# Optimization experiments

Hardware: AMD Instinct MI355X
Metric: run time of the kernel (lower is better)

Reference implementation:

```python
import jax, jax.numpy as jnp
import numpy as np

B_SZ = 16
IN_CH = 4
OUT_CH = 256          # d_model
KSIZE = 16
STRIDE = 8
L_IN = 20000
D_STATE = 128
EXPAND = 2
D_INNER = EXPAND * OUT_CH            # 512
HEADDIM = 64
NHEADS = D_INNER // HEADDIM          # 8
D_CONV = 4
NGROUPS = 1
L_CONV = (L_IN - KSIZE) // STRIDE + 1  # 2499
FLAT = STRIDE * L_CONV                 # 19992 == Config.INPUT_LENGTH
CHUNK = 128
DN = ('NCH', 'OIH', 'NCH')


def setup_inputs() -> dict:
    key = jax.random.key(0)
    ks = jax.random.split(key, 20)
    r = lambda i, shape, s=0.02: jax.random.normal(ks[i], shape, jnp.float32) * s
    return {
        'x': jax.random.normal(ks[0], (B_SZ, IN_CH, L_IN), jnp.float32),
        'conv_w': r(1, (OUT_CH, IN_CH, KSIZE), 0.1),
        'conv_b': r(2, (OUT_CH,), 0.1),
        'bn_w': jnp.ones((OUT_CH,), jnp.float32),
        'bn_b': jnp.zeros((OUT_CH,), jnp.float32),
        'in_proj_w': r(3, (2 * D_INNER + 2 * NGROUPS * D_STATE + NHEADS, OUT_CH)),
        'conv1d_w': r(4, (D_INNER + 2 * NGROUPS * D_STATE, 1, D_CONV), 0.2),
        'conv1d_b': r(5, (D_INNER + 2 * NGROUPS * D_STATE,), 0.1),
        'dt_bias': jnp.linspace(-4.0, -1.0, NHEADS, dtype=jnp.float32),
        'A_log': jnp.log(jnp.arange(1, NHEADS + 1, dtype=jnp.float32)),
        'D': r(6, (NHEADS,), 0.5) + 1.0,
        'norm_w': jnp.ones((D_INNER,), jnp.float32),
        'out_proj_w': r(7, (OUT_CH, D_INNER)),
        'conv1_w': r(8, (STRIDE, OUT_CH, KSIZE), 0.05),
        'conv1_b': r(9, (STRIDE,), 0.1),
        'w1': r(10, (512, FLAT)), 'b1': jnp.zeros((512,), jnp.float32),
        'w2': r(11, (256, 512), 0.05), 'b2': jnp.zeros((256,), jnp.float32),
        'w3': r(12, (64, 256), 0.05), 'b3': jnp.zeros((64,), jnp.float32),
        'w4': r(13, (1, 64), 0.05), 'b4': jnp.zeros((1,), jnp.float32),
    }


def _segsum(a):
    # a: [..., q] -> [..., q, q]; entry (i,j) = sum_{k=j+1..i} a_k on lower triangle
    q = a.shape[-1]
    cs = jnp.cumsum(a, axis=-1)
    seg = cs[..., :, None] - cs[..., None, :]
    mask = jnp.tril(jnp.ones((q, q), dtype=bool))
    return jnp.where(mask, seg, -jnp.inf)


def _ssd(xw, dA, Bm, Cm, chunk):
    # Chunked SSD (Mamba2): xw = dt-weighted inputs [b,l,h,p]; dA = dt*A [b,l,h];
    # Bm, Cm: [b,l,n]. Causal; zero-padding at the tail cannot affect y[:, :l].
    b, l, h, p = xw.shape
    n = Bm.shape[-1]
    pad = (-l) % chunk
    xw = jnp.pad(xw, ((0, 0), (0, pad), (0, 0), (0, 0)))
    dA = jnp.pad(dA, ((0, 0), (0, pad), (0, 0)))
    Bm = jnp.pad(Bm, ((0, 0), (0, pad), (0, 0)))
    Cm = jnp.pad(Cm, ((0, 0), (0, pad), (0, 0)))
    c = (l + pad) // chunk
    xw = xw.reshape(b, c, chunk, h, p)
    dA = dA.reshape(b, c, chunk, h).transpose(0, 3, 1, 2)   # [b,h,c,q]
    Bm = Bm.reshape(b, c, chunk, n)
    Cm = Cm.reshape(b, c, chunk, n)
    Acs = jnp.cumsum(dA, axis=-1)                            # [b,h,c,q]
    Ldiag = jnp.exp(_segsum(dA))                             # [b,h,c,q,q]
    Ydiag = jnp.einsum('bcln,bcsn,bhcls,bcshp->bclhp', Cm, Bm, Ldiag, xw)
    decay_states = jnp.exp(Acs[..., -1:] - Acs)              # [b,h,c,q]
    states = jnp.einsum('bcln,bhcl,bclhp->bchpn', Bm, decay_states, xw)
    chunk_decay = jnp.exp(Acs[..., -1])                      # [b,h,c]

    def step(carry, inp):
        s, d = inp
        return carry * d[..., None, None] + s, carry

    init = jnp.zeros((b, h, p, n), xw.dtype)
    _, prev = jax.lax.scan(step, init,
                           (states.transpose(1, 0, 2, 3, 4),
                            chunk_decay.transpose(2, 0, 1)))
    prev = prev.transpose(1, 0, 2, 3, 4)                     # [b,c,h,p,n]
    Yoff = jnp.einsum('bcln,bchpn,bhcl->bclhp', Cm, prev, jnp.exp(Acs))
    return (Ydiag + Yoff).reshape(b, l + pad, h, p)[:, :l]


def reference(x, conv_w, conv_b, bn_w, bn_b, in_proj_w, conv1d_w, conv1d_b,
              dt_bias, A_log, D, norm_w, out_proj_w, conv1_w, conv1_b,
              w1, b1, w2, b2, w3, b3, w4, b4):
    # conv -> BN (batch stats, training-mode math) -> ReLU
    h = jax.lax.conv_general_dilated(x, conv_w, (STRIDE,), 'VALID',
                                     dimension_numbers=DN) + conv_b[None, :, None]
    mean = h.mean(axis=(0, 2), keepdims=True)
    var = h.var(axis=(0, 2), keepdims=True)
    h = (h - mean) * jax.lax.rsqrt(var + 1e-5)
    h = jax.nn.relu(h * bn_w[None, :, None] + bn_b[None, :, None])
    u = h.transpose(0, 2, 1)                                 # [b, l, d_model]

    # ---- Mamba2 block ----
    zxbcdt = u @ in_proj_w.T                                 # [b, l, 1288]
    z, xBC, dt = jnp.split(zxbcdt, [D_INNER, 2 * D_INNER + 2 * NGROUPS * D_STATE], axis=-1)
    # causal depthwise conv1d over xBC + SiLU
    xBC_t = jnp.pad(xBC.transpose(0, 2, 1), ((0, 0), (0, 0), (D_CONV - 1, 0)))
    xBC_t = jax.lax.conv_general_dilated(xBC_t, conv1d_w, (1,), 'VALID',
                                         dimension_numbers=DN,
                                         feature_group_count=xBC.shape[-1])
    xBC = jax.nn.silu((xBC_t + conv1d_b[None, :, None]).transpose(0, 2, 1))
    xm, Bm, Cm = jnp.split(xBC, [D_INNER, D_INNER + NGROUPS * D_STATE], axis=-1)
    dt = jax.nn.softplus(dt + dt_bias)                       # [b, l, nheads]
    A = -jnp.exp(A_log)                                      # [nheads]
    xh = xm.reshape(xm.shape[0], xm.shape[1], NHEADS, HEADDIM)
    y = _ssd(xh * dt[..., None], dt * A, Bm, Cm, CHUNK)
    y = y + D[None, None, :, None] * xh                      # D skip
    y = y.reshape(y.shape[0], y.shape[1], D_INNER)
    # gated RMSNorm (norm_before_gate=False): rmsnorm(y * silu(z)) * w
    y = y * jax.nn.silu(z)
    y = y * jax.lax.rsqrt(jnp.mean(y * y, axis=-1, keepdims=True) + 1e-5) * norm_w
    y = y @ out_proj_w.T                                     # [b, l, d_model]

    # conv1 with padding='same' (PyTorch: left=(k-1)//2, right=k-1-left)
    h = y.transpose(0, 2, 1)
    pad_l = (KSIZE - 1) // 2
    h = jax.lax.conv_general_dilated(h, conv1_w, (1,), [(pad_l, KSIZE - 1 - pad_l)],
                                     dimension_numbers=DN) + conv1_b[None, :, None]
    f = h.reshape(h.shape[0], -1)                            # [b, 8*2499=19992]
    f = jax.nn.relu(f @ w1.T + b1)
    f = jax.nn.relu(f @ w2.T + b2)
    f = jax.nn.relu(f @ w3.T + b3)
    return f @ w4.T + b4                                     # [b, 1]
```

## Files before the change

kernel.cpp:

```cpp
#include <hip/hip_runtime.h>
#include <math.h>

constexpr int B    = 16;
constexpr int L    = 2499;
constexpr int DIN  = 512;
constexpr int NH   = 8;
constexpr int DS   = 128;
constexpr int NC   = 20;
constexpr int XBCD = 768;
constexpr int FLAT = 19992;
constexpr int FLATP= 20000;
constexpr long ROWS = (long)B * L;

constexpr size_t S_DTV  = 0;
constexpr size_t S_CS   = 1279488;
constexpr size_t S_STAT = 2590208;
constexpr size_t S_WPK  = 2594304;
constexpr size_t S_HALO = 2725376;
constexpr size_t OFF_HT  = 4199936;
constexpr size_t OFF_XBC = 24671744;
constexpr size_t OFF_CBST= 86087168;
constexpr size_t CB_OFF  = 0;
constexpr size_t ST_OFF  = 5242880;
constexpr size_t Z_OFF   = 0;
constexpr size_t F_OFF   = 0;
constexpr size_t O1A_OFF = 640000;
constexpr size_t O1_OFF  = 672768;
constexpr size_t O2_OFF  = 705536;
constexpr size_t O3_OFF  = 721920;
constexpr size_t W1B_OFF = 726016;
constexpr size_t WS_NEEDED = 127030784;

typedef unsigned short u16;
typedef __attribute__((ext_vector_type(8))) short bf16x8;
typedef __attribute__((ext_vector_type(4))) float f32x4;

__device__ __forceinline__ float bf2f(unsigned int u) {
    return __uint_as_float(u << 16);
}
__device__ __forceinline__ u16 f2bf(float f) {
    unsigned int x = __float_as_uint(f);
    unsigned int r = x + 0x7fffu + ((x >> 16) & 1u);
    return (u16)(r >> 16);
}
__device__ __forceinline__ unsigned int pk2(float a, float b) {
    return (unsigned int)f2bf(a) | ((unsigned int)f2bf(b) << 16);
}
__device__ __forceinline__ void ld8bf(const u16* p, float* o) {
    uint4 v = *(const uint4*)p;
    o[0]=bf2f(v.x&0xffffu); o[1]=bf2f(v.x>>16);
    o[2]=bf2f(v.y&0xffffu); o[3]=bf2f(v.y>>16);
    o[4]=bf2f(v.z&0xffffu); o[5]=bf2f(v.z>>16);
    o[6]=bf2f(v.w&0xffffu); o[7]=bf2f(v.w>>16);
}
__device__ __forceinline__ void ld4bf(const u16* p, float* o) {
    uint2 v = *(const uint2*)p;
    o[0]=bf2f(v.x&0xffffu); o[1]=bf2f(v.x>>16);
    o[2]=bf2f(v.y&0xffffu); o[3]=bf2f(v.y>>16);
}
__device__ __forceinline__ void st8bf(u16* p, const float* s) {
    uint4 v;
    v.x = pk2(s[0],s[1]); v.y = pk2(s[2],s[3]);
    v.z = pk2(s[4],s[5]); v.w = pk2(s[6],s[7]);
    *(uint4*)p = v;
}
__device__ __forceinline__ float siluf(float x) { return x / (1.f + expf(-x)); }

__global__ __launch_bounds__(256) void k_zero(float* __restrict__ p, int n) {
    int i = blockIdx.x * 256 + threadIdx.x;
    if (i < n) p[i] = 0.f;
}

__global__ __launch_bounds__(256) void k_wcvt(const float* __restrict__ src,
                                              u16* __restrict__ dst, int n) {
    int i = blockIdx.x * 256 + threadIdx.x;
    if (i < n) dst[i] = f2bf(src[i]);
}

__global__ __launch_bounds__(256) void k_w1cvt(const float* __restrict__ w1,
                                               u16* __restrict__ w1b) {
    long e0 = ((long)blockIdx.x * 256 + threadIdx.x) * 8;
    int n = (int)(e0 / FLATP);
    int k = (int)(e0 - (long)n * FLATP);
    const float* src = w1 + (long)n * FLAT + k;
    u16* dst = w1b + e0;
    if (k + 8 <= FLAT) {
        float4 a = *(const float4*)src;
        float4 b = *(const float4*)(src + 4);
        *(uint4*)dst = (uint4){pk2(a.x,a.y), pk2(a.z,a.w), pk2(b.x,b.y), pk2(b.z,b.w)};
    } else {
        #pragma unroll
        for (int i = 0; i < 8; ++i)
            dst[i] = (k + i < FLAT) ? f2bf(src[i]) : (u16)0;
    }
}

template <bool IM2COL, bool BF16OUT>
__global__ __launch_bounds__(256) void gemm_mfma(const void* __restrict__ Ap,
                                                 const u16* __restrict__ Wb,
                                                 void* __restrict__ Cp,
                                                 int M, int N, int K, int lda, int ldc) {
    __shared__ u16 Als[128 * 40];
    __shared__ u16 Bls[128 * 40];
    int tid = threadIdx.x;
    int wave = tid >> 6, lane = tid & 63;
    int wr = wave >> 1, wc = wave & 1;
    int m0 = blockIdx.x * 128, n0 = blockIdx.y * 128;
    int l15 = lane & 15, l4 = lane >> 4;
    int srow = tid >> 1, scol = (tid & 1) * 16;

    f32x4 acc[4][4];
    #pragma unroll
    for (int i = 0; i < 4; ++i)
        #pragma unroll
        for (int j = 0; j < 4; ++j)
            acc[i][j] = (f32x4){0.f, 0.f, 0.f, 0.f};

    for (int k0 = 0; k0 < K; k0 += 32) {
        {
            int am = m0 + srow;
            uint4 v0 = {0,0,0,0}, v1 = {0,0,0,0};
            if (am < M) {
                if (IM2COL) {
                    const float* x = (const float*)Ap;
                    int b = am / L, l = am - b * L;
                    int ic = (k0 + scol) >> 4;
                    const float* px = x + ((long)(b * 4 + ic)) * 20000 + l * 8;
                    float4 f0 = *(const float4*)(px);
                    float4 f1 = *(const float4*)(px + 4);
                    float4 f2 = *(const float4*)(px + 8);
                    float4 f3 = *(const float4*)(px + 12);
                    v0.x = pk2(f0.x,f0.y); v0.y = pk2(f0.z,f0.w);
                    v0.z = pk2(f1.x,f1.y); v0.w = pk2(f1.z,f1.w);
                    v1.x = pk2(f2.x,f2.y); v1.y = pk2(f2.z,f2.w);
                    v1.z = pk2(f3.x,f3.y); v1.w = pk2(f3.z,f3.w);
                } else {
                    const u16* pa = (const u16*)Ap + (long)am * lda + k0 + scol;
                    v0 = *(const uint4*)pa;
                    v1 = *(const uint4*)(pa + 8);
                }
            }
            *(uint4*)&Als[srow * 40 + scol]     = v0;
            *(uint4*)&Als[srow * 40 + scol + 8] = v1;
        }
        {
            const u16* pw = Wb + (long)(n0 + srow) * K + k0 + scol;
            *(uint4*)&Bls[srow * 40 + scol]     = *(const uint4*)pw;
            *(uint4*)&Bls[srow * 40 + scol + 8] = *(const uint4*)(pw + 8);
        }
        __syncthreads();

        bf16x8 af[4], bfr[4];
        #pragma unroll
        for (int i = 0; i < 4; ++i) {
            af[i]  = *(const bf16x8*)&Als[(wr * 64 + i * 16 + l15) * 40 + l4 * 8];
            bfr[i] = *(const bf16x8*)&Bls[(wc * 64 + i * 16 + l15) * 40 + l4 * 8];
        }
        #pragma unroll
        for (int i = 0; i < 4; ++i)
            #pragma unroll
            for (int j = 0; j < 4; ++j)
                acc[i][j] = __builtin_amdgcn_mfma_f32_16x16x32_bf16(
                    af[i], bfr[j], acc[i][j], 0, 0, 0);
        __syncthreads();
    }

    #pragma unroll
    for (int i = 0; i < 4; ++i) {
        #pragma unroll
        for (int j = 0; j < 4; ++j) {
            int n = n0 + wc * 64 + j * 16 + l15;
            #pragma unroll
            for (int r = 0; r < 4; ++r) {
                int m = m0 + wr * 64 + i * 16 + l4 * 4 + r;
                if (m < M) {
                    if (BF16OUT) ((u16*)Cp)[(long)m * ldc + n] = f2bf(acc[i][j][r]);
                    else         ((float*)Cp)[(long)m * ldc + n] = acc[i][j][r];
                }
            }
        }
    }
}

__global__ __launch_bounds__(256) void k_bnstats(const u16* __restrict__ h,
                                                 float* __restrict__ sums,
                                                 float* __restrict__ sumsq) {
    int c = threadIdx.x;
    float s = 0.f, s2 = 0.f;
    for (long r = blockIdx.x; r < ROWS; r += gridDim.x) {
        float v = bf2f(h[r * 256 + c]);
        s += v; s2 += v * v;
    }
    atomicAdd(&sums[c], s);
    atomicAdd(&sumsq[c], s2);
}

__global__ __launch_bounds__(256) void k_bnfinal(const float* __restrict__ sums,
                                                 const float* __restrict__ sumsq,
                                                 const float* __restrict__ bn_w,
                                                 const float* __restrict__ bn_b,
                                                 float* __restrict__ scale,
                                                 float* __restrict__ shift) {
    int c = threadIdx.x;
    float mean = sums[c] / (float)ROWS;
    float var  = sumsq[c] / (float)ROWS - mean * mean;
    float inv  = rsqrtf(var + 1e-5f);
    float sc   = bn_w[c] * inv;
    scale[c] = sc;
    shift[c] = bn_b[c] - mean * sc;
}

__global__ __launch_bounds__(256) void k_bnapply(u16* __restrict__ ht,
                                                 const float* __restrict__ scale,
                                                 const float* __restrict__ shift) {
    long i = ((long)blockIdx.x * 256 + threadIdx.x) * 8;
    int c = (int)(i & 255);
    float v[8];
    ld8bf(ht + i, v);
    float4 s0 = *(const float4*)(scale + c), s1 = *(const float4*)(scale + c + 4);
    float4 h0 = *(const float4*)(shift + c), h1 = *(const float4*)(shift + c + 4);
    v[0]=fmaxf(fmaf(v[0],s0.x,h0.x),0.f); v[1]=fmaxf(fmaf(v[1],s0.y,h0.y),0.f);
    v[2]=fmaxf(fmaf(v[2],s0.z,h0.z),0.f); v[3]=fmaxf(fmaf(v[3],s0.w,h0.w),0.f);
    v[4]=fmaxf(fmaf(v[4],s1.x,h1.x),0.f); v[5]=fmaxf(fmaf(v[5],s1.y,h1.y),0.f);
    v[6]=fmaxf(fmaf(v[6],s1.z,h1.z),0.f); v[7]=fmaxf(fmaf(v[7],s1.w,h1.w),0.f);
    st8bf(ht + i, v);
}

__global__ __launch_bounds__(256) void k_dtproj(const u16* __restrict__ u,
                                                const float* __restrict__ in_proj_w,
                                                const float* __restrict__ dt_bias,
                                                float* __restrict__ dtv) {
    long idx = (long)blockIdx.x * 256 + threadIdx.x;
    if (idx >= ROWS * 8) return;
    int h = (int)(idx & 7);
    long row = idx >> 3;
    const float* wr = in_proj_w + (long)(1280 + h) * 256;
    const u16* ar = u + row * 256;
    float acc = dt_bias[h];
    for (int k = 0; k < 256; ++k)
        acc = fmaf(bf2f(ar[k]), wr[k], acc);
    dtv[idx] = (acc > 20.f) ? acc : log1pf(expf(acc));
}

__global__ __launch_bounds__(256) void k_halo(const u16* __restrict__ xbc,
                                              u16* __restrict__ halo) {
    long idx = (long)blockIdx.x * 256 + threadIdx.x;
    if (idx >= 16L * 19 * 3 * 768) return;
    int ch = (int)(idx % 768);
    long t1 = idx / 768;
    int j = (int)(t1 % 3);
    long t2 = t1 / 3;
    int t = (int)(t2 % 19) + 1;
    int b = (int)(t2 / 19);
    halo[(((long)b * 20 + t) * 3 + j) * 768 + ch] =
        xbc[((long)b * L + t * 128 - 3 + j) * 768 + ch];
}

__global__ __launch_bounds__(256) void k_dwip(u16* __restrict__ xbc,
                                              const u16* __restrict__ halo,
                                              const float* __restrict__ w,
                                              const float* __restrict__ bias) {
    int cg = blockIdx.x % 3;
    int t  = (blockIdx.x / 3) % 20;
    int b  = blockIdx.x / 60;
    int ch = cg * 256 + threadIdx.x;
    int l0 = t * 128, l1 = min(l0 + 128, L);
    float W0 = w[ch*4+0], W1 = w[ch*4+1], W2 = w[ch*4+2], W3 = w[ch*4+3];
    float bs = bias[ch];
    float p0 = 0.f, p1 = 0.f, p2 = 0.f;
    if (t > 0) {
        const u16* hp = halo + (((long)b * 20 + t) * 3) * 768 + ch;
        p0 = bf2f(hp[0]); p1 = bf2f(hp[768]); p2 = bf2f(hp[1536]);
    }
    u16* base = xbc + ((long)b * L + l0) * 768 + ch;
    for (int l = l0; l < l1; ++l) {
        float p3 = bf2f(*base);
        float acc = fmaf(p0, W0, fmaf(p1, W1, fmaf(p2, W2, fmaf(p3, W3, bs))));
        *base = f2bf(siluf(acc));
        p0 = p1; p1 = p2; p2 = p3;
        base += 768;
    }
}

__global__ __launch_bounds__(128) void k_cs(const float* __restrict__ dtv,
                                            const float* __restrict__ A_log,
                                            float* __restrict__ cs) {
    int c = blockIdx.x % NC;
    int h = (blockIdx.x / NC) % NH;
    int b = blockIdx.x / (NC * NH);
    int q = threadIdx.x;
    int lg = c * 128 + q;
    float Av = -expf(A_log[h]);
    float dA = 0.f;
    if (lg < L) dA = dtv[((long)b * L + lg) * 8 + h] * Av;
    __shared__ float buf[128];
    buf[q] = dA;
    __syncthreads();
    for (int off = 1; off < 128; off <<= 1) {
        float add = (q >= off) ? buf[q - off] : 0.f;
        __syncthreads();
        buf[q] += add;
        __syncthreads();
    }
    cs[(long)blockIdx.x * 128 + q] = buf[q];
}

__global__ __launch_bounds__(256) void k_cb(const u16* __restrict__ xbc,
                                            u16* __restrict__ cb, int bo) {
    int c = blockIdx.x % NC, bl = blockIdx.x / NC;
    int b = bo + bl;
    long bcl = blockIdx.x;
    __shared__ u16 Als[128 * 40];
    __shared__ u16 Bls[128 * 40];
    int tid = threadIdx.x;
    int wave = tid >> 6, lane = tid & 63;
    int wr = wave >> 1, wc = wave & 1;
    int l15 = lane & 15, l4 = lane >> 4;
    int srow = tid >> 1, scol = (tid & 1) * 16;

    f32x4 acc[4][4];
    #pragma unroll
    for (int i = 0; i < 4; ++i)
        #pragma unroll
        for (int j = 0; j < 4; ++j)
            acc[i][j] = (f32x4){0.f, 0.f, 0.f, 0.f};

    int lg = c * 128 + srow;
    const u16* prow = xbc + ((long)b * L + lg) * XBCD;

    for (int k0 = 0; k0 < 128; k0 += 32) {
        uint4 cv0 = {0,0,0,0}, cv1 = cv0, bv0 = cv0, bv1 = cv0;
        if (lg < L) {
            cv0 = *(const uint4*)(prow + 640 + k0 + scol);
            cv1 = *(const uint4*)(prow + 640 + k0 + scol + 8);
            bv0 = *(const uint4*)(prow + 512 + k0 + scol);
            bv1 = *(const uint4*)(prow + 512 + k0 + scol + 8);
        }
        *(uint4*)&Als[srow * 40 + scol]     = cv0;
        *(uint4*)&Als[srow * 40 + scol + 8] = cv1;
        *(uint4*)&Bls[srow * 40 + scol]     = bv0;
        *(uint4*)&Bls[srow * 40 + scol + 8] = bv1;
        __syncthreads();

        bf16x8 af[4], bfr[4];
        #pragma unroll
        for (int i = 0; i < 4; ++i) {
            af[i]  = *(const bf16x8*)&Als[(wr * 64 + i * 16 + l15) * 40 + l4 * 8];
            bfr[i] = *(const bf16x8*)&Bls[(wc * 64 + i * 16 + l15) * 40 + l4 * 8];
        }
        #pragma unroll
        for (int i = 0; i < 4; ++i)
            #pragma unroll
            for (int j = 0; j < 4; ++j)
                acc[i][j] = __builtin_amdgcn_mfma_f32_16x16x32_bf16(
                    af[i], bfr[j], acc[i][j], 0, 0, 0);
        __syncthreads();
    }

    #pragma unroll
    for (int i = 0; i < 4; ++i)
        #pragma unroll
        for (int j = 0; j < 4; ++j) {
            int n = wc * 64 + j * 16 + l15;
            #pragma unroll
            for (int r = 0; r < 4; ++r) {
                int m = wr * 64 + i * 16 + l4 * 4 + r;
                cb[(bcl * 128 + m) * 128 + n] = f2bf(acc[i][j][r]);
            }
        }
}

__global__ __launch_bounds__(256) void k_states(const u16* __restrict__ xbc,
                                                const float* __restrict__ dtv,
                                                const float* __restrict__ cs,
                                                u16* __restrict__ st, int bo) {
    int h = blockIdx.x & 7;
    int c = (blockIdx.x >> 3) % NC;
    int bl = blockIdx.x / (8 * NC);
    int b = bo + bl;
    __shared__ u16 At[128][136];
    __shared__ u16 Bt[64][136];
    long csbase = (((long)b * 8 + h) * NC + c) * 128;
    float csLast = cs[csbase + 127];
    int tid = threadIdx.x;
    int lane = tid & 63, wave = tid >> 6;
    int wr = wave >> 1, wc = wave & 1;
    int l15 = lane & 15, l4 = lane >> 4;

    int l0 = 2 * (tid & 63), l1 = l0 + 1;
    int q = tid >> 6;
    int lg0 = c * 128 + l0, lg1 = c * 128 + l1;
    long row0 = (long)b * L + lg0, row1 = row0 + 1;
    float wl0 = 0.f, wl1 = 0.f, dt0 = 0.f, dt1 = 0.f;
    if (lg0 < L) { wl0 = expf(csLast - cs[csbase + l0]); dt0 = dtv[row0 * 8 + h]; }
    if (lg1 < L) { wl1 = expf(csLast - cs[csbase + l1]); dt1 = dtv[row1 * 8 + h]; }

    #pragma unroll
    for (int nb = 0; nb < 4; ++nb) {
        int n0 = q * 32 + nb * 8;
        float a0[8] = {0,0,0,0,0,0,0,0}, a1[8] = {0,0,0,0,0,0,0,0};
        if (lg0 < L) ld8bf(xbc + row0 * XBCD + 512 + n0, a0);
        if (lg1 < L) ld8bf(xbc + row1 * XBCD + 512 + n0, a1);
        #pragma unroll
        for (int i = 0; i < 8; ++i)
            *(unsigned int*)&At[n0 + i][l0] = pk2(a0[i] * wl0, a1[i] * wl1);
    }
    #pragma unroll
    for (int pb = 0; pb < 2; ++pb) {
        int p0 = q * 16 + pb * 8;
        float a0[8] = {0,0,0,0,0,0,0,0}, a1[8] = {0,0,0,0,0,0,0,0};
        if (lg0 < L) ld8bf(xbc + row0 * XBCD + h * 64 + p0, a0);
        if (lg1 < L) ld8bf(xbc + row1 * XBCD + h * 64 + p0, a1);
        #pragma unroll
        for (int i = 0; i < 8; ++i)
            *(unsigned int*)&Bt[p0 + i][l0] = pk2(a0[i] * dt0, a1[i] * dt1);
    }
    __syncthreads();

    f32x4 acc[4][2];
    #pragma unroll
    for (int i = 0; i < 4; ++i)
        #pragma unroll
        for (int j = 0; j < 2; ++j)
            acc[i][j] = (f32x4){0.f, 0.f, 0.f, 0.f};

    #pragma unroll
    for (int k0 = 0; k0 < 128; k0 += 32) {
        bf16x8 af[4], bfr[2];
        #pragma unroll
        for (int i = 0; i < 4; ++i)
            af[i] = *(const bf16x8*)&At[wr * 64 + i * 16 + l15][k0 + l4 * 8];
        #pragma unroll
        for (int j = 0; j < 2; ++j)
            bfr[j] = *(const bf16x8*)&Bt[wc * 32 + j * 16 + l15][k0 + l4 * 8];
        #pragma unroll
        for (int i = 0; i < 4; ++i)
            #pragma unroll
            for (int j = 0; j < 2; ++j)
                acc[i][j] = __builtin_amdgcn_mfma_f32_16x16x32_bf16(
                    af[i], bfr[j], acc[i][j], 0, 0, 0);
    }

    long basep = (long)blockIdx.x * 8192;
    #pragma unroll
    for (int i = 0; i < 4; ++i)
        #pragma unroll
        for (int j = 0; j < 2; ++j) {
            int p = wc * 32 + j * 16 + l15;
            #pragma unroll
            for (int r = 0; r < 4; ++r) {
                int n = wr * 64 + i * 16 + l4 * 4 + r;
                st[basep + n * 64 + p] = f2bf(acc[i][j][r]);
            }
        }
}

__global__ __launch_bounds__(256) void k_scan(const float* __restrict__ cs,
                                              u16* __restrict__ st, int bo) {
    int h = blockIdx.x & 7, bl = (blockIdx.x >> 3) & 7, q = blockIdx.x >> 6;
    int b = bo + bl;
    int tid = threadIdx.x;
    float carry[8];
    #pragma unroll
    for (int i = 0; i < 8; ++i) carry[i] = 0.f;
    long csbase = ((long)b * 8 + h) * NC * 128;
    for (int c = 0; c < NC; ++c) {
        float cd = expf(cs[csbase + c * 128 + 127]);
        u16* p = st + (((long)bl * NC + c) * 8 + h) * 8192 + q * 2048;
        #pragma unroll
        for (int i = 0; i < 8; ++i) {
            int e = tid + i * 256;
            float v = bf2f(p[e]);
            p[e] = f2bf(carry[i]);
            carry[i] = carry[i] * cd + v;
        }
    }
}

__global__ __launch_bounds__(256) void k_yout(u16* __restrict__ xbc,
                                              const float* __restrict__ dtv,
                                              const float* __restrict__ cs,
                                              const u16* __restrict__ cb,
                                              const u16* __restrict__ st,
                                              const float* __restrict__ Dv, int bo) {
    int h = blockIdx.x & 7;
    int c = (blockIdx.x >> 3) % NC;
    int bl = blockIdx.x / (8 * NC);
    int b = bo + bl;
    long bcl = (long)bl * NC + c;
    __shared__ u16 Am[128][136];
    __shared__ u16 Bt[64][136];
    __shared__ float csb[128], ecs[128];
    int tid = threadIdx.x;
    long csbase = (((long)b * 8 + h) * NC + c) * 128;
    if (tid < 128) {
        float v = cs[csbase + tid];
        csb[tid] = v;
        ecs[tid] = expf(v);
    }
    __syncthreads();

    int lane = tid & 63, wave = tid >> 6;
    int wr = wave >> 1, wc = wave & 1;
    int l15 = lane & 15, l4 = lane >> 4;
    int lrow = tid >> 1, sh = (tid & 1) * 64;
    int l0 = 2 * (tid & 63), l1 = l0 + 1;
    int q = tid >> 6;
    int lg0 = c * 128 + l0, lg1 = c * 128 + l1;
    long row0 = (long)b * L + lg0, row1 = row0 + 1;

    {
        float cl = csb[lrow];
        const u16* cbrow = cb + (bcl * 128 + lrow) * 128;
        #pragma unroll
        for (int sb = 0; sb < 8; ++sb) {
            int s0 = sh + sb * 8;
            float a[8];
            ld8bf(cbrow + s0, a);
            #pragma unroll
            for (int i = 0; i < 8; ++i) {
                int s = s0 + i;
                float w = (s <= lrow) ? expf(cl - csb[s]) : 0.f;
                a[i] *= w;
            }
            st8bf(&Am[lrow][s0], a);
        }
        float dt0 = 0.f, dt1 = 0.f;
        if (lg0 < L) dt0 = dtv[row0 * 8 + h];
        if (lg1 < L) dt1 = dtv[row1 * 8 + h];
        #pragma unroll
        for (int pb = 0; pb < 2; ++pb) {
            int p0 = q * 16 + pb * 8;
            float a0[8] = {0,0,0,0,0,0,0,0}, a1[8] = {0,0,0,0,0,0,0,0};
            if (lg0 < L) ld8bf(xbc + row0 * XBCD + h * 64 + p0, a0);
            if (lg1 < L) ld8bf(xbc + row1 * XBCD + h * 64 + p0, a1);
            #pragma unroll
            for (int i = 0; i < 8; ++i)
                *(unsigned int*)&Bt[p0 + i][l0] = pk2(a0[i] * dt0, a1[i] * dt1);
        }
    }
    __syncthreads();

    f32x4 acc[4][2];
    #pragma unroll
    for (int i = 0; i < 4; ++i)
        #pragma unroll
        for (int j = 0; j < 2; ++j)
            acc[i][j] = (f32x4){0.f, 0.f, 0.f, 0.f};

    #pragma unroll
    for (int k0 = 0; k0 < 128; k0 += 32) {
        bf16x8 af[4], bfr[2];
        #pragma unroll
        for (int i = 0; i < 4; ++i)
            af[i] = *(const bf16x8*)&Am[wr * 64 + i * 16 + l15][k0 + l4 * 8];
        #pragma unroll
        for (int j = 0; j < 2; ++j)
            bfr[j] = *(const bf16x8*)&Bt[wc * 32 + j * 16 + l15][k0 + l4 * 8];
        #pragma unroll
        for (int i = 0; i < 4; ++i)
            #pragma unroll
            for (int j = 0; j < 2; ++j)
                acc[i][j] = __builtin_amdgcn_mfma_f32_16x16x32_bf16(
                    af[i], bfr[j], acc[i][j], 0, 0, 0);
    }
    __syncthreads();

    {
        float el = ecs[lrow];
        int lgr = c * 128 + lrow;
        const u16* xr = xbc + ((long)b * L + lgr) * XBCD + 640;
        #pragma unroll
        for (int nb = 0; nb < 8; ++nb) {
            int n0 = sh + nb * 8;
            float a[8] = {0,0,0,0,0,0,0,0};
            if (lgr < L) {
                ld8bf(xr + n0, a);
                #pragma unroll
                for (int i = 0; i < 8; ++i) a[i] *= el;
            }
            st8bf(&Am[lrow][n0], a);
        }
        const u16* pv = st + (bcl * 8 + h) * 8192;
        #pragma unroll
        for (int pb = 0; pb < 2; ++pb) {
            int p0 = q * 16 + pb * 8;
            float a0[8], a1[8];
            ld8bf(pv + (long)l0 * 64 + p0, a0);
            ld8bf(pv + (long)l1 * 64 + p0, a1);
            #pragma unroll
            for (int i = 0; i < 8; ++i)
                *(unsigned int*)&Bt[p0 + i][l0] = pk2(a0[i], a1[i]);
        }
    }
    __syncthreads();

    #pragma unroll
    for (int k0 = 0; k0 < 128; k0 += 32) {
        bf16x8 af[4], bfr[2];
        #pragma unroll
        for (int i = 0; i < 4; ++i)
            af[i] = *(const bf16x8*)&Am[wr * 64 + i * 16 + l15][k0 + l4 * 8];
        #pragma unroll
        for (int j = 0; j < 2; ++j)
            bfr[j] = *(const bf16x8*)&Bt[wc * 32 + j * 16 + l15][k0 + l4 * 8];
        #pragma unroll
        for (int i = 0; i < 4; ++i)
            #pragma unroll
            for (int j = 0; j < 2; ++j)
                acc[i][j] = __builtin_amdgcn_mfma_f32_16x16x32_bf16(
                    af[i], bfr[j], acc[i][j], 0, 0, 0);
    }

    float Dh = Dv[h];
    #pragma unroll
    for (int i = 0; i < 4; ++i)
        #pragma unroll
        for (int r = 0; r < 4; ++r) {
            int l = wr * 64 + i * 16 + l4 * 4 + r;
            int lg = c * 128 + l;
            if (lg >= L) continue;
            long row = (long)b * L + lg;
            #pragma unroll
            for (int j = 0; j < 2; ++j) {
                int p = wc * 32 + j * 16 + l15;
                u16* xp = xbc + row * XBCD + h * 64 + p;
                float xv = bf2f(*xp);
                *xp = f2bf(fmaf(Dh, xv, acc[i][j][r]));
            }
        }
}

__global__ __launch_bounds__(256) void k_rmsnorm(u16* __restrict__ y,
                                                 const u16* __restrict__ z,
                                                 const float* __restrict__ nw) {
    long r = blockIdx.x;
    int tid = threadIdx.x;
    float v0 = bf2f(y[r * XBCD + tid]), v1 = bf2f(y[r * XBCD + 256 + tid]);
    float z0 = bf2f(z[r * DIN + tid]),  z1 = bf2f(z[r * DIN + 256 + tid]);
    v0 *= siluf(z0);
    v1 *= siluf(z1);
    __shared__ float red[256];
    red[tid] = v0 * v0 + v1 * v1;
    __syncthreads();
    for (int s = 128; s > 0; s >>= 1) {
        if (tid < s) red[tid] += red[tid + s];
        __syncthreads();
    }
    float sc = rsqrtf(red[0] / 512.f + 1e-5f);
    y[r * XBCD + tid]       = f2bf(v0 * sc * nw[tid]);
    y[r * XBCD + 256 + tid] = f2bf(v1 * sc * nw[256 + tid]);
}

__global__ __launch_bounds__(256) void k_wpack(const float* __restrict__ w,
                                               u16* __restrict__ wp) {
    int idx = blockIdx.x * 256 + threadIdx.x;
    if (idx >= 8 * 256 * 16) return;
    int k = idx & 15;
    int cidx = (idx >> 4) & 255;
    int s = idx >> 12;
    wp[(s * 16 + k) * 256 + cidx] = f2bf(w[idx]);
}

__global__ __launch_bounds__(256) void k_conv1(const u16* __restrict__ G,
                                               const float* __restrict__ bias,
                                               u16* __restrict__ f) {
    long idx = (long)blockIdx.x * 256 + threadIdx.x;
    if (idx >= (long)B * 8 * L) {
        long j = idx - (long)B * 8 * L;
        if (j < 16 * 8)
            f[(j >> 3) * FLATP + FLAT + (j & 7)] = 0;
        return;
    }
    int l = (int)(idx % L);
    long t = idx / L;
    int s = (int)(t & 7);
    int b = (int)(t >> 3);
    float acc = bias[s];
    #pragma unroll
    for (int k = 0; k < 16; ++k) {
        int ls = l + k - 7;
        if (ls >= 0 && ls < L)
            acc += bf2f(G[((long)b * L + ls) * 128 + s * 16 + k]);
    }
    f[(long)b * FLATP + s * L + l] = f2bf(acc);
}

__global__ __launch_bounds__(256) void k_mlp1(const u16* __restrict__ fb,
                                              const u16* __restrict__ w1b,
                                              float* __restrict__ o1acc) {
    int wave = threadIdx.x >> 6, lane = threadIdx.x & 63;
    int l15 = lane & 15, l4 = lane >> 4;
    int n0 = blockIdx.x * 64 + wave * 16;
    int k0 = blockIdx.y * 800;
    const u16* fp = fb + (long)l15 * FLATP + k0 + l4 * 8;
    const u16* wp = w1b + (long)(n0 + l15) * FLATP + k0 + l4 * 8;
    f32x4 acc = (f32x4){0.f, 0.f, 0.f, 0.f};
    #pragma unroll
    for (int kk = 0; kk < 25; ++kk) {
        bf16x8 af = *(const bf16x8*)fp;
        bf16x8 bf = *(const bf16x8*)wp;
        acc = __builtin_amdgcn_mfma_f32_16x16x32_bf16(af, bf, acc, 0, 0, 0);
        fp += 32; wp += 32;
    }
    #pragma unroll
    for (int r = 0; r < 4; ++r) {
        int b = l4 * 4 + r;
        atomicAdd(&o1acc[b * 512 + n0 + l15], acc[r]);
    }
}

__global__ __launch_bounds__(256) void k_mlp1fin(const float* __restrict__ o1acc,
                                                 const float* __restrict__ b1,
                                                 float* __restrict__ o1) {
    int i = blockIdx.x * 256 + threadIdx.x;
    o1[i] = fmaxf(o1acc[i] + b1[i & 511], 0.f);
}

__global__ __launch_bounds__(256) void k_mlp2(const float* __restrict__ in,
                                              const float* __restrict__ w,
                                              const float* __restrict__ bias,
                                              float* __restrict__ out) {
    int b = blockIdx.x, n = threadIdx.x;
    const float* ir = in + b * 512;
    const float* wr = w + (long)n * 512;
    float acc = 0.f;
    for (int k = 0; k < 512; ++k) acc = fmaf(ir[k], wr[k], acc);
    out[b * 256 + n] = fmaxf(acc + bias[n], 0.f);
}

__global__ __launch_bounds__(64) void k_mlp3(const float* __restrict__ in,
                                             const float* __restrict__ w,
                                             const float* __restrict__ bias,
                                             float* __restrict__ out) {
    int b = blockIdx.x, n = threadIdx.x;
    const float* ir = in + b * 256;
    const float* wr = w + (long)n * 256;
    float acc = 0.f;
    for (int k = 0; k < 256; ++k) acc = fmaf(ir[k], wr[k], acc);
    out[b * 64 + n] = fmaxf(acc + bias[n], 0.f);
}

__global__ __launch_bounds__(64) void k_mlp4(const float* __restrict__ in,
                                             const float* __restrict__ w4,
                                             const float* __restrict__ b4,
                                             float* __restrict__ dout) {
    int b = blockIdx.x, k = threadIdx.x;
    float v = in[b * 64 + k] * w4[k];
    #pragma unroll
    for (int off = 32; off > 0; off >>= 1) v += __shfl_down(v, off);
    if (k == 0) dout[b] = v + b4[0];
}

extern "C" void kernel_launch(void* const* d_in, const int* in_sizes, int n_in,
                              void* d_out, int out_size, void* d_ws, size_t ws_size,
                              hipStream_t stream) {
    (void)in_sizes; (void)n_in; (void)out_size;
    if (ws_size < WS_NEEDED) return;

    const float* x         = (const float*)d_in[0];
    const float* conv_w    = (const float*)d_in[1];
    const float* bn_w      = (const float*)d_in[3];
    const float* bn_b      = (const float*)d_in[4];
    const float* in_proj_w = (const float*)d_in[5];
    const float* conv1d_w  = (const float*)d_in[6];
    const float* conv1d_b  = (const float*)d_in[7];
    const float* dt_bias   = (const float*)d_in[8];
    const float* A_log     = (const float*)d_in[9];
    const float* Dp        = (const float*)d_in[10];
    const float* norm_w    = (const float*)d_in[11];
    const float* out_proj_w= (const float*)d_in[12];
    const float* conv1_w   = (const float*)d_in[13];
    const float* conv1_b   = (const float*)d_in[14];
    const float* w1 = (const float*)d_in[15]; const float* b1 = (const float*)d_in[16];
    const float* w2 = (const float*)d_in[17]; const float* b2 = (const float*)d_in[18];
    const float* w3 = (const float*)d_in[19]; const float* b3 = (const float*)d_in[20];
    const float* w4 = (const float*)d_in[21]; const float* b4 = (const float*)d_in[22];

    char* base = (char*)d_ws;
    float* dtv  = (float*)(base + S_DTV);
    float* cs   = (float*)(base + S_CS);
    float* sums = (float*)(base + S_STAT);
    float* sumsq= sums + 256;
    float* scale= sums + 512;
    float* shift= sums + 768;
    u16*   cwbf = (u16*)(base + S_WPK);
    u16*   wbf  = (u16*)(base + S_HALO);
    u16*   halo = (u16*)(base + S_HALO);
    u16*   ht   = (u16*)(base + OFF_HT);
    u16*   xbc  = (u16*)(base + OFF_XBC);
    u16*   cb   = (u16*)(base + OFF_CBST + CB_OFF);
    u16*   st   = (u16*)(base + OFF_CBST + ST_OFF);
    u16*   zb   = (u16*)(base + OFF_CBST + Z_OFF);
    u16*   G    = (u16*)(base + OFF_XBC);
    u16*   fbuf = (u16*)(base + OFF_CBST + F_OFF);
    float* o1a  = (float*)(base + OFF_CBST + O1A_OFF);
    float* o1   = (float*)(base + OFF_CBST + O1_OFF);
    float* o2   = (float*)(base + OFF_CBST + O2_OFF);
    float* o3   = (float*)(base + OFF_CBST + O3_OFF);
    u16*   w1b  = (u16*)(base + OFF_CBST + W1B_OFF);
    u16*   yproj= ht;

    k_wcvt<<<64, 256, 0, stream>>>(conv_w, cwbf, 256 * 64);
    gemm_mfma<true, true><<<dim3(313, 2), 256, 0, stream>>>(
        x, cwbf, ht, (int)ROWS, 256, 64, 0, 256);

    k_zero<<<2, 256, 0, stream>>>(sums, 512);
    k_bnstats<<<256, 256, 0, stream>>>(ht, sums, sumsq);
    k_bnfinal<<<1, 256, 0, stream>>>(sums, sumsq, bn_w, bn_b, scale, shift);
    k_bnapply<<<4998, 256, 0, stream>>>(ht, scale, shift);

    k_wcvt<<<768, 256, 0, stream>>>(in_proj_w + 512L * 256, wbf, 768 * 256);
    gemm_mfma<false, true><<<dim3(313, 6), 256, 0, stream>>>(
        ht, wbf, xbc, (int)ROWS, 768, 256, 256, 768);
    k_dtproj<<<1250, 256, 0, stream>>>(ht, in_proj_w, dt_bias, dtv);

    k_halo<<<2736, 256, 0, stream>>>(xbc, halo);
    k_dwip<<<960, 256, 0, stream>>>(xbc, halo, conv1d_w, conv1d_b);
    k_cs<<<2560, 128, 0, stream>>>(dtv, A_log, cs);

    for (int bh = 0; bh < 2; ++bh) {
        int bo = bh * 8;
        k_cb<<<160, 256, 0, stream>>>(xbc, cb, bo);
        k_states<<<1280, 256, 0, stream>>>(xbc, dtv, cs, st, bo);
        k_scan<<<256, 256, 0, stream>>>(cs, st, bo);
        k_yout<<<1280, 256, 0, stream>>>(xbc, dtv, cs, cb, st, Dp, bo);
    }

    k_wcvt<<<512, 256, 0, stream>>>(in_proj_w, wbf, 512 * 256);
    gemm_mfma<false, true><<<dim3(313, 4), 256, 0, stream>>>(
        ht, wbf, zb, (int)ROWS, 512, 256, 256, 512);

    k_rmsnorm<<<39984, 256, 0, stream>>>(xbc, zb, norm_w);
    k_wcvt<<<512, 256, 0, stream>>>(out_proj_w, wbf, 256 * 512);
    gemm_mfma<false, true><<<dim3(313, 2), 256, 0, stream>>>(
        xbc, wbf, yproj, (int)ROWS, 256, 512, 768, 256);

    k_wpack<<<128, 256, 0, stream>>>(conv1_w, wbf);
    gemm_mfma<false, true><<<dim3(313, 1), 256, 0, stream>>>(
        yproj, wbf, G, (int)ROWS, 128, 256, 256, 128);
    k_conv1<<<1250, 256, 0, stream>>>(G, conv1_b, fbuf);

    k_w1cvt<<<5000, 256, 0, stream>>>(w1, w1b);
    k_zero<<<32, 256, 0, stream>>>(o1a, 8192);
    k_mlp1<<<dim3(8, 25), 256, 0, stream>>>(fbuf, w1b, o1a);
    k_mlp1fin<<<32, 256, 0, stream>>>(o1a, b1, o1);
    k_mlp2<<<16, 256, 0, stream>>>(o1, w2, b2, o2);
    k_mlp3<<<16, 64, 0, stream>>>(o2, w3, b3, o3);
    k_mlp4<<<16, 64, 0, stream>>>(o3, w4, b4, (float*)d_out);
}
```

Before: 709.9 us.

## Halve SSD shared tiles via K-split, use exp2 cumsums, wave-per-row RMSNorm

```diff
diff --git a/kernel.cpp b/kernel.cpp
--- a/kernel.cpp
+++ b/kernel.cpp
@@ -11,6 +11,7 @@
 constexpr int FLAT = 19992;
 constexpr int FLATP= 20000;
 constexpr long ROWS = (long)B * L;
+constexpr float LOG2E = 1.4426950408889634f;
 
 constexpr size_t S_DTV  = 0;
 constexpr size_t S_CS   = 1279488;
@@ -302,7 +303,7 @@
         buf[q] += add;
         __syncthreads();
     }
-    cs[(long)blockIdx.x * 128 + q] = buf[q];
+    cs[(long)blockIdx.x * 128 + q] = buf[q] * LOG2E;
 }
 
 __global__ __launch_bounds__(256) void k_cb(const u16* __restrict__ xbc,
@@ -378,44 +379,15 @@
     int c = (blockIdx.x >> 3) % NC;
     int bl = blockIdx.x / (8 * NC);
     int b = bo + bl;
-    __shared__ u16 At[128][136];
-    __shared__ u16 Bt[64][136];
+    __shared__ u16 At[128][72];
+    __shared__ u16 Bt[64][72];
     long csbase = (((long)b * 8 + h) * NC + c) * 128;
-    float csLast = cs[csbase + 127];
+    float cs2Last = cs[csbase + 127];
     int tid = threadIdx.x;
     int lane = tid & 63, wave = tid >> 6;
     int wr = wave >> 1, wc = wave & 1;
     int l15 = lane & 15, l4 = lane >> 4;
-
-    int l0 = 2 * (tid & 63), l1 = l0 + 1;
-    int q = tid >> 6;
-    int lg0 = c * 128 + l0, lg1 = c * 128 + l1;
-    long row0 = (long)b * L + lg0, row1 = row0 + 1;
-    float wl0 = 0.f, wl1 = 0.f, dt0 = 0.f, dt1 = 0.f;
-    if (lg0 < L) { wl0 = expf(csLast - cs[csbase + l0]); dt0 = dtv[row0 * 8 + h]; }
-    if (lg1 < L) { wl1 = expf(csLast - cs[csbase + l1]); dt1 = dtv[row1 * 8 + h]; }
-
-    #pragma unroll
-    for (int nb = 0; nb < 4; ++nb) {
-        int n0 = q * 32 + nb * 8;
-        float a0[8] = {0,0,0,0,0,0,0,0}, a1[8] = {0,0,0,0,0,0,0,0};
-        if (lg0 < L) ld8bf(xbc + row0 * XBCD + 512 + n0, a0);
-        if (lg1 < L) ld8bf(xbc + row1 * XBCD + 512 + n0, a1);
-        #pragma unroll
-        for (int i = 0; i < 8; ++i)
-            *(unsigned int*)&At[n0 + i][l0] = pk2(a0[i] * wl0, a1[i] * wl1);
-    }
-    #pragma unroll
-    for (int pb = 0; pb < 2; ++pb) {
-        int p0 = q * 16 + pb * 8;
-        float a0[8] = {0,0,0,0,0,0,0,0}, a1[8] = {0,0,0,0,0,0,0,0};
-        if (lg0 < L) ld8bf(xbc + row0 * XBCD + h * 64 + p0, a0);
-        if (lg1 < L) ld8bf(xbc + row1 * XBCD + h * 64 + p0, a1);
-        #pragma unroll
-        for (int i = 0; i < 8; ++i)
-            *(unsigned int*)&Bt[p0 + i][l0] = pk2(a0[i] * dt0, a1[i] * dt1);
-    }
-    __syncthreads();
+    int pr = tid & 31, grp = tid >> 5;
 
     f32x4 acc[4][2];
     #pragma unroll
@@ -425,20 +397,52 @@
             acc[i][j] = (f32x4){0.f, 0.f, 0.f, 0.f};
 
     #pragma unroll
-    for (int k0 = 0; k0 < 128; k0 += 32) {
-        bf16x8 af[4], bfr[2];
-        #pragma unroll
-        for (int i = 0; i < 4; ++i)
-            af[i] = *(const bf16x8*)&At[wr * 64 + i * 16 + l15][k0 + l4 * 8];
-        #pragma unroll
-        for (int j = 0; j < 2; ++j)
-            bfr[j] = *(const bf16x8*)&Bt[wc * 32 + j * 16 + l15][k0 + l4 * 8];
-        #pragma unroll
-        for (int i = 0; i < 4; ++i)
+    for (int lh = 0; lh < 2; ++lh) {
+        int l0 = lh * 64 + 2 * pr, l1 = l0 + 1;
+        int lg0 = c * 128 + l0, lg1 = lg0 + 1;
+        long row0 = (long)b * L + lg0, row1 = row0 + 1;
+        float wl0 = 0.f, wl1 = 0.f, dt0 = 0.f, dt1 = 0.f;
+        if (lg0 < L) { wl0 = exp2f(cs2Last - cs[csbase + l0]); dt0 = dtv[row0 * 8 + h]; }
+        if (lg1 < L) { wl1 = exp2f(cs2Last - cs[csbase + l1]); dt1 = dtv[row1 * 8 + h]; }
+
+        #pragma unroll
+        for (int nb = 0; nb < 2; ++nb) {
+            int n0 = grp * 16 + nb * 8;
+            float a0[8] = {0,0,0,0,0,0,0,0}, a1[8] = {0,0,0,0,0,0,0,0};
+            if (lg0 < L) ld8bf(xbc + row0 * XBCD + 512 + n0, a0);
+            if (lg1 < L) ld8bf(xbc + row1 * XBCD + 512 + n0, a1);
+            #pragma unroll
+            for (int i = 0; i < 8; ++i)
+                *(unsigned int*)&At[n0 + i][2 * pr] = pk2(a0[i] * wl0, a1[i] * wl1);
+        }
+        {
+            int p0 = grp * 8;
+            float a0[8] = {0,0,0,0,0,0,0,0}, a1[8] = {0,0,0,0,0,0,0,0};
+            if (lg0 < L) ld8bf(xbc + row0 * XBCD + h * 64 + p0, a0);
+            if (lg1 < L) ld8bf(xbc + row1 * XBCD + h * 64 + p0, a1);
+            #pragma unroll
+            for (int i = 0; i < 8; ++i)
+                *(unsigned int*)&Bt[p0 + i][2 * pr] = pk2(a0[i] * dt0, a1[i] * dt1);
+        }
+        __syncthreads();
+
+        #pragma unroll
+        for (int k0 = 0; k0 < 64; k0 += 32) {
+            bf16x8 af[4], bfr[2];
+            #pragma unroll
+            for (int i = 0; i < 4; ++i)
+                af[i] = *(const bf16x8*)&At[wr * 64 + i * 16 + l15][k0 + l4 * 8];
             #pragma unroll
             for (int j = 0; j < 2; ++j)
-                acc[i][j] = __builtin_amdgcn_mfma_f32_16x16x32_bf16(
-                    af[i], bfr[j], acc[i][j], 0, 0, 0);
+                bfr[j] = *(const bf16x8*)&Bt[wc * 32 + j * 16 + l15][k0 + l4 * 8];
+            #pragma unroll
+            for (int i = 0; i < 4; ++i)
+                #pragma unroll
+                for (int j = 0; j < 2; ++j)
+                    acc[i][j] = __builtin_amdgcn_mfma_f32_16x16x32_bf16(
+                        af[i], bfr[j], acc[i][j], 0, 0, 0);
+        }
+        __syncthreads();
     }
 
     long basep = (long)blockIdx.x * 8192;
@@ -465,7 +469,7 @@
     for (int i = 0; i < 8; ++i) carry[i] = 0.f;
     long csbase = ((long)b * 8 + h) * NC * 128;
     for (int c = 0; c < NC; ++c) {
-        float cd = expf(cs[csbase + c * 128 + 127]);
+        float cd = exp2f(cs[csbase + c * 128 + 127]);
         u16* p = st + (((long)bl * NC + c) * 8 + h) * 8192 + q * 2048;
         #pragma unroll
         for (int i = 0; i < 8; ++i) {
@@ -488,128 +492,132 @@
     int bl = blockIdx.x / (8 * NC);
     int b = bo + bl;
     long bcl = (long)bl * NC + c;
-    __shared__ u16 Am[128][136];
-    __shared__ u16 Bt[64][136];
+    __shared__ u16 Am[128][72];
+    __shared__ u16 Bt[64][72];
     __shared__ float csb[128], ecs[128];
     int tid = threadIdx.x;
     long csbase = (((long)b * 8 + h) * NC + c) * 128;
     if (tid < 128) {
         float v = cs[csbase + tid];
         csb[tid] = v;
-        ecs[tid] = expf(v);
+        ecs[tid] = exp2f(v);
     }
     __syncthreads();
 
     int lane = tid & 63, wave = tid >> 6;
     int wr = wave >> 1, wc = wave & 1;
     int l15 = lane & 15, l4 = lane >> 4;
-    int lrow = tid >> 1, sh = (tid & 1) * 64;
-    int l0 = 2 * (tid & 63), l1 = l0 + 1;
-    int q = tid >> 6;
-    int lg0 = c * 128 + l0, lg1 = c * 128 + l1;
-    long row0 = (long)b * L + lg0, row1 = row0 + 1;
-
-    {
-        float cl = csb[lrow];
-        const u16* cbrow = cb + (bcl * 128 + lrow) * 128;
-        #pragma unroll
-        for (int sb = 0; sb < 8; ++sb) {
-            int s0 = sh + sb * 8;
-            float a[8];
-            ld8bf(cbrow + s0, a);
-            #pragma unroll
-            for (int i = 0; i < 8; ++i) {
-                int s = s0 + i;
-                float w = (s <= lrow) ? expf(cl - csb[s]) : 0.f;
-                a[i] *= w;
+    int lrow = tid >> 1, sh32 = (tid & 1) * 32;
+    int pr = tid & 31, grp = tid >> 5;
+
+    f32x4 acc[4][2];
+    #pragma unroll
+    for (int i = 0; i < 4; ++i)
+        #pragma unroll
+        for (int j = 0; j < 2; ++j)
+            acc[i][j] = (f32x4){0.f, 0.f, 0.f, 0.f};
+
+    #pragma unroll
+    for (int sh2 = 0; sh2 < 2; ++sh2) {
+        int sbase = sh2 * 64;
+        {
+            float cl = csb[lrow];
+            const u16* cbrow = cb + (bcl * 128 + lrow) * 128 + sbase + sh32;
+            #pragma unroll
+            for (int sb = 0; sb < 4; ++sb) {
+                float a[8];
+                ld8bf(cbrow + sb * 8, a);
+                #pragma unroll
+                for (int i = 0; i < 8; ++i) {
+                    int s = sbase + sh32 + sb * 8 + i;
+                    float w = (s <= lrow) ? exp2f(cl - csb[s]) : 0.f;
+                    a[i] *= w;
+                }
+                st8bf(&Am[lrow][sh32 + sb * 8], a);
             }
-            st8bf(&Am[lrow][s0], a);
-        }
-        float dt0 = 0.f, dt1 = 0.f;
-        if (lg0 < L) dt0 = dtv[row0 * 8 + h];
-        if (lg1 < L) dt1 = dtv[row1 * 8 + h];
-        #pragma unroll
-        for (int pb = 0; pb < 2; ++pb) {
-            int p0 = q * 16 + pb * 8;
+        }
+        {
+            int l0 = sbase + 2 * pr, l1 = l0 + 1;
+            int lg0 = c * 128 + l0, lg1 = lg0 + 1;
+            long row0 = (long)b * L + lg0, row1 = row0 + 1;
+            float dt0 = 0.f, dt1 = 0.f;
+            if (lg0 < L) dt0 = dtv[row0 * 8 + h];
+            if (lg1 < L) dt1 = dtv[row1 * 8 + h];
+            int p0 = grp * 8;
             float a0[8] = {0,0,0,0,0,0,0,0}, a1[8] = {0,0,0,0,0,0,0,0};
             if (lg0 < L) ld8bf(xbc + row0 * XBCD + h * 64 + p0, a0);
             if (lg1 < L) ld8bf(xbc + row1 * XBCD + h * 64 + p0, a1);
             #pragma unroll
             for (int i = 0; i < 8; ++i)
-                *(unsigned int*)&Bt[p0 + i][l0] = pk2(a0[i] * dt0, a1[i] * dt1);
-        }
-    }
-    __syncthreads();
-
-    f32x4 acc[4][2];
-    #pragma unroll
-    for (int i = 0; i < 4; ++i)
-        #pragma unroll
-        for (int j = 0; j < 2; ++j)
-            acc[i][j] = (f32x4){0.f, 0.f, 0.f, 0.f};
-
-    #pragma unroll
-    for (int k0 = 0; k0 < 128; k0 += 32) {
-        bf16x8 af[4], bfr[2];
-        #pragma unroll
-        for (int i = 0; i < 4; ++i)
-            af[i] = *(const bf16x8*)&Am[wr * 64 + i * 16 + l15][k0 + l4 * 8];
-        #pragma unroll
-        for (int j = 0; j < 2; ++j)
-            bfr[j] = *(const bf16x8*)&Bt[wc * 32 + j * 16 + l15][k0 + l4 * 8];
-        #pragma unroll
-        for (int i = 0; i < 4; ++i)
+                *(unsigned int*)&Bt[p0 + i][2 * pr] = pk2(a0[i] * dt0, a1[i] * dt1);
+        }
+        __syncthreads();
+        #pragma unroll
+        for (int k0 = 0; k0 < 64; k0 += 32) {
+            bf16x8 af[4], bfr[2];
+            #pragma unroll
+            for (int i = 0; i < 4; ++i)
+                af[i] = *(const bf16x8*)&Am[wr * 64 + i * 16 + l15][k0 + l4 * 8];
             #pragma unroll
             for (int j = 0; j < 2; ++j)
-                acc[i][j] = __builtin_amdgcn_mfma_f32_16x16x32_bf16(
-                    af[i], bfr[j], acc[i][j], 0, 0, 0);
-    }
-    __syncthreads();
-
-    {
-        float el = ecs[lrow];
-        int lgr = c * 128 + lrow;
-        const u16* xr = xbc + ((long)b * L + lgr) * XBCD + 640;
-        #pragma unroll
-        for (int nb = 0; nb < 8; ++nb) {
-            int n0 = sh + nb * 8;
-            float a[8] = {0,0,0,0,0,0,0,0};
-            if (lgr < L) {
-                ld8bf(xr + n0, a);
+                bfr[j] = *(const bf16x8*)&Bt[wc * 32 + j * 16 + l15][k0 + l4 * 8];
+            #pragma unroll
+            for (int i = 0; i < 4; ++i)
                 #pragma unroll
-                for (int i = 0; i < 8; ++i) a[i] *= el;
+                for (int j = 0; j < 2; ++j)
+                    acc[i][j] = __builtin_amdgcn_mfma_f32_16x16x32_bf16(
+                        af[i], bfr[j], acc[i][j], 0, 0, 0);
+        }
+        __syncthreads();
+    }
+
+    #pragma unroll
+    for (int nh2 = 0; nh2 < 2; ++nh2) {
+        int nbase = nh2 * 64;
+        {
+            float el = ecs[lrow];
+            int lgr = c * 128 + lrow;
+            const u16* xr = xbc + ((long)b * L + lgr) * XBCD + 640 + nbase + sh32;
+            #pragma unroll
+            for (int sb = 0; sb < 4; ++sb) {
+                float a[8] = {0,0,0,0,0,0,0,0};
+                if (lgr < L) {
+                    ld8bf(xr + sb * 8, a);
+                    #pragma unroll
+                    for (int i = 0; i < 8; ++i) a[i] *= el;
+                }
+                st8bf(&Am[lrow][sh32 + sb * 8], a);
             }
-            st8bf(&Am[lrow][n0], a);
-        }
-        const u16* pv = st + (bcl * 8 + h) * 8192;
-        #pragma unroll
-        for (int pb = 0; pb < 2; ++pb) {
-            int p0 = q * 16 + pb * 8;
+        }
+        {
+            int n0 = nbase + 2 * pr;
+            const u16* pv = st + (bcl * 8 + h) * 8192;
+            int p0 = grp * 8;
             float a0[8], a1[8];
-            ld8bf(pv + (long)l0 * 64 + p0, a0);
-            ld8bf(pv + (long)l1 * 64 + p0, a1);
+            ld8bf(pv + (long)n0 * 64 + p0, a0);
+            ld8bf(pv + (long)(n0 + 1) * 64 + p0, a1);
             #pragma unroll
             for (int i = 0; i < 8; ++i)
-                *(unsigned int*)&Bt[p0 + i][l0] = pk2(a0[i], a1[i]);
-        }
-    }
-    __syncthreads();
-
-    #pragma unroll
-    for (int k0 = 0; k0 < 128; k0 += 32) {
-        bf16x8 af[4], bfr[2];
-        #pragma unroll
-        for (int i = 0; i < 4; ++i)
-            af[i] = *(const bf16x8*)&Am[wr * 64 + i * 16 + l15][k0 + l4 * 8];
-        #pragma unroll
-        for (int j = 0; j < 2; ++j)
-            bfr[j] = *(const bf16x8*)&Bt[wc * 32 + j * 16 + l15][k0 + l4 * 8];
-        #pragma unroll
-        for (int i = 0; i < 4; ++i)
+                *(unsigned int*)&Bt[p0 + i][2 * pr] = pk2(a0[i], a1[i]);
+        }
+        __syncthreads();
+        #pragma unroll
+        for (int k0 = 0; k0 < 64; k0 += 32) {
+            bf16x8 af[4], bfr[2];
+            #pragma unroll
+            for (int i = 0; i < 4; ++i)
+                af[i] = *(const bf16x8*)&Am[wr * 64 + i * 16 + l15][k0 + l4 * 8];
             #pragma unroll
             for (int j = 0; j < 2; ++j)
-                acc[i][j] = __builtin_amdgcn_mfma_f32_16x16x32_bf16(
-                    af[i], bfr[j], acc[i][j], 0, 0, 0);
+                bfr[j] = *(const bf16x8*)&Bt[wc * 32 + j * 16 + l15][k0 + l4 * 8];
+            #pragma unroll
+            for (int i = 0; i < 4; ++i)
+                #pragma unroll
+                for (int j = 0; j < 2; ++j)
+                    acc[i][j] = __builtin_amdgcn_mfma_f32_16x16x32_bf16(
+                        af[i], bfr[j], acc[i][j], 0, 0, 0);
+        }
+        __syncthreads();
     }
 
     float Dh = Dv[h];
@@ -634,22 +642,26 @@
 __global__ __launch_bounds__(256) void k_rmsnorm(u16* __restrict__ y,
                                                  const u16* __restrict__ z,
                                                  const float* __restrict__ nw) {
-    long r = blockIdx.x;
-    int tid = threadIdx.x;
-    float v0 = bf2f(y[r * XBCD + tid]), v1 = bf2f(y[r * XBCD + 256 + tid]);
-    float z0 = bf2f(z[r * DIN + tid]),  z1 = bf2f(z[r * DIN + 256 + tid]);
-    v0 *= siluf(z0);
-    v1 *= siluf(z1);
-    __shared__ float red[256];
-    red[tid] = v0 * v0 + v1 * v1;
-    __syncthreads();
-    for (int s = 128; s > 0; s >>= 1) {
-        if (tid < s) red[tid] += red[tid + s];
-        __syncthreads();
-    }
-    float sc = rsqrtf(red[0] / 512.f + 1e-5f);
-    y[r * XBCD + tid]       = f2bf(v0 * sc * nw[tid]);
-    y[r * XBCD + 256 + tid] = f2bf(v1 * sc * nw[256 + tid]);
+    int wave = threadIdx.x >> 6, lane = threadIdx.x & 63;
+    long r = (long)blockIdx.x * 4 + wave;
+    int c0 = lane * 8;
+    float v[8], zv[8];
+    ld8bf(y + r * XBCD + c0, v);
+    ld8bf(z + r * DIN + c0, zv);
+    float ss = 0.f;
+    #pragma unroll
+    for (int j = 0; j < 8; ++j) {
+        v[j] *= siluf(zv[j]);
+        ss += v[j] * v[j];
+    }
+    #pragma unroll
+    for (int off = 32; off > 0; off >>= 1) ss += __shfl_xor(ss, off, 64);
+    float sc = rsqrtf(ss / 512.f + 1e-5f);
+    float4 w0 = *(const float4*)(nw + c0);
+    float4 w1 = *(const float4*)(nw + c0 + 4);
+    v[0] *= sc * w0.x; v[1] *= sc * w0.y; v[2] *= sc * w0.z; v[3] *= sc * w0.w;
+    v[4] *= sc * w1.x; v[5] *= sc * w1.y; v[6] *= sc * w1.z; v[7] *= sc * w1.w;
+    st8bf(y + r * XBCD + c0, v);
 }
 
 __global__ __launch_bounds__(256) void k_wpack(const float* __restrict__ w,
@@ -831,7 +843,7 @@
     gemm_mfma<false, true><<<dim3(313, 4), 256, 0, stream>>>(
         ht, wbf, zb, (int)ROWS, 512, 256, 256, 512);
 
-    k_rmsnorm<<<39984, 256, 0, stream>>>(xbc, zb, norm_w);
+    k_rmsnorm<<<9996, 256, 0, stream>>>(xbc, zb, norm_w);
     k_wcvt<<<512, 256, 0, stream>>>(out_proj_w, wbf, 256 * 512);
     gemm_mfma<false, true><<<dim3(313, 2), 256, 0, stream>>>(
         xbc, wbf, yproj, (int)ROWS, 256, 512, 768, 256);
```

Result: faster. 669.9 us (-5.6%).
